# Kernel optimization log

Hardware: AMD Instinct MI355X
Metric: run time of the kernel (lower is better)

## Reference

```python
import jax, jax.numpy as jnp
import numpy as np

R = 16            # DFL bins (reg_max)
C = 80            # num classes
STRIDES = (8, 16, 32)
CONF = 0.25
IOU_T = 0.45
MAX_DET = 300
K_PRE = 1024      # fixed pre-NMS candidate count (static-shape stand-in for torch's boolean mask)
CLS_OFFSET = 4096.0  # > max image coord; class-aware NMS offset (torchvision batched_nms trick)


def setup_inputs() -> dict:
    key = jax.random.key(0)
    k0, k1, k2 = jax.random.split(key, 3)
    B, CH = 16, 4 * R + C
    return {
        "p0": jax.random.normal(k0, (B, CH, 80, 80), jnp.float32),
        "p1": jax.random.normal(k1, (B, CH, 40, 40), jnp.float32),
        "p2": jax.random.normal(k2, (B, CH, 20, 20), jnp.float32),
        "h_img": 640,
        "w_img": 640,
    }


def _decode_level(p, stride):
    # p: (B, 4R+C, H, W)
    B, _, H, W = p.shape
    box_logits = p[:, : 4 * R].reshape(B, 4, R, H * W)
    bins = jnp.arange(R, dtype=p.dtype)
    # DFLIntegral: softmax over bins, expectation -> l,t,r,b distances (in stride units)
    ltrb = jnp.einsum('bkrm,r->bkm', jax.nn.softmax(box_logits, axis=2), bins) * stride  # (B,4,HW)
    yv, xv = jnp.meshgrid(jnp.arange(H, dtype=p.dtype), jnp.arange(W, dtype=p.dtype), indexing='ij')
    cx = (xv.reshape(-1) + 0.5) * stride  # (HW,)
    cy = (yv.reshape(-1) + 0.5) * stride
    x1 = cx[None] - ltrb[:, 0]
    y1 = cy[None] - ltrb[:, 1]
    x2 = cx[None] + ltrb[:, 2]
    y2 = cy[None] + ltrb[:, 3]
    boxes = jnp.stack((x1, y1, x2, y2), axis=2)  # (B, HW, 4)
    scores = jax.nn.sigmoid(p[:, 4 * R:].reshape(B, C, H * W))  # (B, C, HW)
    smax = scores.max(axis=1)      # (B, HW)
    labels = scores.argmax(axis=1)  # (B, HW) int
    return boxes, smax, labels


def _pairwise_iou(b):
    # b: (K, 4) xyxy
    area = (b[:, 2] - b[:, 0]) * (b[:, 3] - b[:, 1])
    lt = jnp.maximum(b[:, None, :2], b[None, :, :2])
    rb = jnp.minimum(b[:, None, 2:], b[None, :, 2:])
    wh = jnp.clip(rb - lt, 0.0)
    inter = wh[..., 0] * wh[..., 1]
    return inter / (area[:, None] + area[None, :] - inter + 1e-7)


def _nms_single(boxes, smax, labels):
    # boxes (A,4), smax (A,), labels (A,)
    s = jnp.where(smax > CONF, smax, -1.0)
    sv, idx = jax.lax.top_k(s, K_PRE)          # score-sorted pre-NMS candidates
    bsel = boxes[idx]                           # (K,4)
    lsel = labels[idx]
    vsel = sv > CONF                            # candidate passes conf filter
    boff = bsel + lsel[:, None].astype(bsel.dtype) * CLS_OFFSET  # class-aware offset
    iou = _pairwise_iou(boff)
    iou = iou * (1.0 - jnp.eye(K_PRE, dtype=iou.dtype))  # no self-suppression

    def step(supp, i):
        keep_i = jnp.logical_and(~supp[i], vsel[i])
        supp = jnp.where(keep_i, supp | (iou[i] > IOU_T), supp)
        return supp, keep_i

    _, keep = jax.lax.scan(step, jnp.zeros(K_PRE, bool), jnp.arange(K_PRE))
    rank = jnp.cumsum(keep) - 1
    slot = jnp.where(keep & (rank < MAX_DET), rank, MAX_DET)  # dump overflow into dummy slot
    boxes_out = jnp.zeros((MAX_DET + 1, 4), bsel.dtype).at[slot].set(bsel)[:MAX_DET]
    scores_out = jnp.zeros((MAX_DET + 1,), sv.dtype).at[slot].set(sv)[:MAX_DET]
    labels_out = jnp.full((MAX_DET + 1,), -1, jnp.int32).at[slot].set(lsel.astype(jnp.int32))[:MAX_DET]
    n = jnp.minimum(keep.sum(), MAX_DET)
    valid_out = jnp.arange(MAX_DET) < n
    return boxes_out, scores_out, labels_out, valid_out


def reference(p0, p1, p2, h_img, w_img):
    parts = [_decode_level(p, s) for p, s in zip((p0, p1, p2), STRIDES)]
    boxes = jnp.concatenate([x[0] for x in parts], axis=1)   # (B, A, 4)
    smax = jnp.concatenate([x[1] for x in parts], axis=1)    # (B, A)
    labels = jnp.concatenate([x[2] for x in parts], axis=1)  # (B, A)
    hi = jnp.array([w_img - 1, h_img - 1, w_img - 1, h_img - 1], boxes.dtype)
    boxes = jnp.clip(boxes, 0.0, hi)
    return jax.vmap(_nms_single)(boxes, smax, labels)
```

## Files before the change

kernel.cpp:

```cpp
#include <hip/hip_runtime.h>
#include <stdint.h>

#define NR 16
#define NC 80
#define NA 8400
#define NB 16
#define KPRE 1024
#define MAXDET 300
#define CONF_T 0.25f
#define IOU_THR 0.45f

__device__ __forceinline__ float read_dim(const void* p) {
  int iv = *(const int*)p;
  return (iv > 0 && iv < (1 << 20)) ? (float)iv : *(const float*)p;
}

__device__ __forceinline__ const float* level_ptr(const float* p0, const float* p1,
                                                  const float* p2, int a, int& HW,
                                                  int& W, float& stride, int& m) {
  if (a < 6400)      { HW = 6400; W = 80; stride = 8.f;  m = a;        return p0; }
  else if (a < 8000) { HW = 1600; W = 40; stride = 16.f; m = a - 6400; return p1; }
  else               { HW = 400;  W = 20; stride = 32.f; m = a - 8000; return p2; }
}

__device__ __forceinline__ uint64_t readlane64(uint64_t v, int lane) {
  uint32_t lo = (uint32_t)__builtin_amdgcn_readlane((int)(uint32_t)v, lane);
  uint32_t hi = (uint32_t)__builtin_amdgcn_readlane((int)(uint32_t)(v >> 32), lane);
  return ((uint64_t)hi << 32) | lo;
}

__global__ __launch_bounds__(64) void k_decode(
    const float* __restrict__ p0, const float* __restrict__ p1,
    const float* __restrict__ p2, const void* __restrict__ hp,
    const void* __restrict__ wp, float4* __restrict__ boxes,
    uint32_t* __restrict__ keys, int* __restrict__ labels) {
  int aid = blockIdx.x * 64 + threadIdx.x;
  int b = aid / NA, a = aid - b * NA;
  int HW, W, m; float stride;
  const float* p = level_ptr(p0, p1, p2, a, HW, W, stride, m);
  const float* base = p + (size_t)b * (4 * NR + NC) * HW + m;

  float d[4];
#pragma unroll
  for (int k = 0; k < 4; ++k) {
    const float* bk = base + (size_t)(k * NR) * HW;
    float v[NR]; float mx = -3.4e38f;
#pragma unroll
    for (int r = 0; r < NR; ++r) { v[r] = bk[(size_t)r * HW]; mx = fmaxf(mx, v[r]); }
    float se = 0.f, sn = 0.f;
#pragma unroll
    for (int r = 0; r < NR; ++r) { float e = expf(v[r] - mx); se += e; sn += e * (float)r; }
    d[k] = sn / se * stride;
  }

  const float* bc = base + (size_t)(4 * NR) * HW;
  float ml = -3.4e38f; int mc = NC;
#pragma unroll 8
  for (int ch = 0; ch < NC; ++ch) {
    float vv = bc[(size_t)ch * HW];
    if (vv > ml) { ml = vv; mc = ch; }
  }

  int y = m / W, x = m - y * W;
  float cx = ((float)x + 0.5f) * stride, cy = ((float)y + 0.5f) * stride;
  float hx = read_dim(wp) - 1.f, hy = read_dim(hp) - 1.f;
  boxes[aid] = make_float4(fminf(fmaxf(cx - d[0], 0.f), hx),
                           fminf(fmaxf(cy - d[1], 0.f), hy),
                           fminf(fmaxf(cx + d[2], 0.f), hx),
                           fminf(fmaxf(cy + d[3], 0.f), hy));
  float smax = 1.f / (1.f + expf(-ml));
  float s = smax > CONF_T ? smax : -1.0f;
  uint32_t bt = __float_as_uint(s);
  keys[aid] = (bt & 0x80000000u) ? ~bt : (bt | 0x80000000u);
  labels[aid] = mc;
}

__global__ __launch_bounds__(1024) void k_selcomp(const uint32_t* __restrict__ keys,
                                                  uint64_t* __restrict__ cmp,
                                                  int* __restrict__ ccount) {
  __shared__ __align__(16) uint32_t skeys[NA];
  __shared__ uint32_t whist[16][256];
  __shared__ uint32_t hsum[256], ssuf[256];
  __shared__ int s_b1, s_rem, s_t16, s_cnt;
  int img = blockIdx.x, tid = threadIdx.x;
  int w = tid >> 6, lane = tid & 63;
  const uint4* kb4 = (const uint4*)(keys + (size_t)img * NA);
  for (int j = tid; j < NA / 4; j += 1024) ((uint4*)skeys)[j] = kb4[j];
  if (tid == 0) s_cnt = 0;

  for (int j = tid; j < 16 * 256; j += 1024) ((uint32_t*)whist)[j] = 0;
  __syncthreads();
  for (int j = tid; j < NA; j += 1024) atomicAdd(&whist[w][skeys[j] >> 24], 1u);
  __syncthreads();
  if (tid < 256) { uint32_t s = 0; for (int i = 0; i < 16; ++i) s += whist[i][tid]; hsum[tid] = s; }
  __syncthreads();
  if (tid < 256) { uint32_t s = 0; for (int j = tid; j < 256; ++j) s += hsum[j]; ssuf[tid] = s; }
  __syncthreads();
  if (tid < 256) {
    uint32_t ab = (tid == 255) ? 0u : ssuf[tid + 1];
    if (ssuf[tid] >= KPRE && ab < KPRE) { s_b1 = tid; s_rem = KPRE - (int)ab; }
  }
  __syncthreads();
  int b1 = s_b1, rem = s_rem;
  __syncthreads();

  for (int j = tid; j < 16 * 256; j += 1024) ((uint32_t*)whist)[j] = 0;
  __syncthreads();
  for (int j = tid; j < NA; j += 1024) {
    uint32_t k = skeys[j];
    if ((int)(k >> 24) == b1) atomicAdd(&whist[w][(k >> 16) & 0xFF], 1u);
  }
  __syncthreads();
  if (tid < 256) { uint32_t s = 0; for (int i = 0; i < 16; ++i) s += whist[i][tid]; hsum[tid] = s; }
  __syncthreads();
  if (tid < 256) { uint32_t s = 0; for (int j = tid; j < 256; ++j) s += hsum[j]; ssuf[tid] = s; }
  __syncthreads();
  if (tid < 256) {
    int ab = (tid == 255) ? 0 : (int)ssuf[tid + 1];
    if ((int)ssuf[tid] >= rem && ab < rem) s_t16 = (b1 << 8) | tid;
  }
  __syncthreads();
  uint32_t t16 = (uint32_t)s_t16;

  for (int j0 = 0; j0 < NA; j0 += 1024) {
    int j = j0 + tid;
    uint32_t k = (j < NA) ? skeys[j] : 0;
    bool pass = (j < NA) && ((k >> 16) >= t16);
    uint64_t mask = __ballot(pass);
    int pre = __popcll(mask & ((1ull << lane) - 1ull));
    int wc = __popcll(mask);
    int base = 0;
    if (lane == 0) base = wc ? atomicAdd(&s_cnt, wc) : 0;
    base = __shfl(base, 0);
    if (pass)
      cmp[(size_t)img * NA + base + pre] =
          ((uint64_t)k << 32) | (uint64_t)(0xFFFFFFFFu - (uint32_t)j);
  }
  __syncthreads();
  if (tid == 0) ccount[img] = s_cnt;
}

__global__ __launch_bounds__(256) void k_rank2(
    const uint64_t* __restrict__ cmp, const int* __restrict__ ccount,
    const float4* __restrict__ boxes, const int* __restrict__ labels,
    float4* __restrict__ selbox, float4* __restrict__ selboff,
    float* __restrict__ selscore, int* __restrict__ sellab) {
  __shared__ uint64_t sk[2048];
  int img = blockIdx.y;
  int M = ccount[img]; if (M > NA) M = NA;
  if (blockIdx.x * 256 >= M) return;
  int c = blockIdx.x * 256 + threadIdx.x;
  uint64_t kc = (c < M) ? cmp[(size_t)img * NA + c] : 0;
  int rank = 0;
  for (int j0 = 0; j0 < M; j0 += 2048) {
    int nchunk = min(2048, M - j0);
    __syncthreads();
    for (int j = threadIdx.x; j < nchunk; j += 256)
      sk[j] = cmp[(size_t)img * NA + j0 + j];
    __syncthreads();
    if (c < M) {
      int j = 0;
      for (; j + 4 <= nchunk; j += 4) {
        rank += (int)(sk[j] > kc) + (int)(sk[j + 1] > kc) +
                (int)(sk[j + 2] > kc) + (int)(sk[j + 3] > kc);
      }
      for (; j < nchunk; ++j) rank += (int)(sk[j] > kc);
    }
  }
  if (c < M && rank < KPRE) {
    int a = (int)(0xFFFFFFFFu - (uint32_t)kc);
    uint32_t uk = (uint32_t)(kc >> 32);
    uint32_t bits = (uk & 0x80000000u) ? (uk & 0x7FFFFFFFu) : ~uk;
    float s = __uint_as_float(bits);
    int lab = labels[img * NA + a];
    float4 bx = boxes[img * NA + a];
    float off = (float)lab * 4096.0f;
    int o = img * KPRE + rank;
    selbox[o] = bx;
    selboff[o] = make_float4(bx.x + off, bx.y + off, bx.z + off, bx.w + off);
    selscore[o] = s;
    sellab[o] = lab;
  }
}

__global__ __launch_bounds__(256) void k_iou(const float4* __restrict__ selboff,
                                             uint64_t* __restrict__ rowmask) {
  __shared__ float4 bb[KPRE];
  __shared__ float sar[KPRE];
  int img = blockIdx.y;
  for (int j = threadIdx.x; j < KPRE; j += 256) {
    float4 v = selboff[img * KPRE + j];
    bb[j] = v;
    sar[j] = (v.z - v.x) * (v.w - v.y);
  }
  __syncthreads();
  int i = blockIdx.x * 16 + (threadIdx.x & 15);
  int w = threadIdx.x >> 4;
  int rot = w & 3;
  float4 bi = bb[i];
  float ai = sar[i];
  uint64_t bits = 0;
  for (int jj = 0; jj < 64; ++jj) {
    int jb = (jj + rot) & 63;
    int j = w * 64 + jb;
    float4 bj = bb[j];
    float lx = fmaxf(bi.x, bj.x), ly = fmaxf(bi.y, bj.y);
    float rx = fminf(bi.z, bj.z), ry = fminf(bi.w, bj.w);
    float iw = fmaxf(rx - lx, 0.f), ih = fmaxf(ry - ly, 0.f);
    float inter = iw * ih;
    float aj = sar[j];
    float iou = inter / (ai + aj - inter + 1e-7f);
    bits |= (uint64_t)((iou > IOU_THR) && (j != i)) << jb;
  }
  rowmask[(size_t)img * 16384 + (size_t)w * 1024 + i] = bits;
}

__global__ __launch_bounds__(64) void k_scan(
    const uint64_t* __restrict__ rowmask, const float4* __restrict__ selbox,
    const float* __restrict__ selscore, const int* __restrict__ sellab,
    float* __restrict__ out) {
  __shared__ float lsc[KPRE];
  __shared__ uint64_t buf[2][16 * 65];
  __shared__ int keepidx[MAXDET];
  int img = blockIdx.x, lane = threadIdx.x;
  int wsel = lane & 15, q = lane >> 4;
  const uint64_t* g = rowmask + (size_t)img * 16384;

  for (int j = lane; j < KPRE; j += 64) lsc[j] = selscore[img * KPRE + j];

  {
    uint64_t r0[16];
#pragma unroll
    for (int t = 0; t < 16; ++t) r0[t] = g[t * 1024 + lane];
#pragma unroll
    for (int t = 0; t < 16; ++t) buf[0][t * 65 + lane] = r0[t];
  }
  asm volatile("" ::: "memory");

  uint64_t remv = 0;
  int n = 0;
  for (int c = 0; c < 16; ++c) {
    uint64_t rn[16];
    if (c + 1 < 16) {
#pragma unroll
      for (int t = 0; t < 16; ++t) rn[t] = g[t * 1024 + (c + 1) * 64 + lane];
    }
    const uint64_t* B = buf[c & 1];
    uint64_t m = B[c * 65 + lane];
    float sc = lsc[c * 64 + lane];
    uint64_t vmask = __ballot(sc > CONF_T);
    uint64_t cur = readlane64(remv, c) | readlane64(remv, c + 16) |
                   readlane64(remv, c + 32) | readlane64(remv, c + 48);
    uint64_t kmask = 0;
#pragma unroll
    for (int ii = 0; ii < 64; ++ii) {
      if (((vmask >> ii) & 1ull) && !((cur >> ii) & 1ull)) {
        cur |= readlane64(m, ii);
        kmask |= (1ull << ii);
        if (lane == 0 && n < MAXDET) keepidx[n] = c * 64 + ii;
        n++;
      }
    }
    {
      uint64_t acc = 0;
#pragma unroll
      for (int t = 0; t < 16; ++t) {
        int ii = q * 16 + t;
        uint64_t msk = (uint64_t)0 - ((kmask >> ii) & 1ull);
        acc |= B[wsel * 65 + ii] & msk;
      }
      remv |= acc;
    }
    if (!((vmask >> 63) & 1ull) || n >= MAXDET) break;
    if (c + 1 < 16) {
#pragma unroll
      for (int t = 0; t < 16; ++t) buf[(c + 1) & 1][t * 65 + lane] = rn[t];
    }
    asm volatile("" ::: "memory");
  }

  asm volatile("" ::: "memory");
  float* ob = out;
  float* os = out + NB * MAXDET * 4;
  float* ol = out + NB * MAXDET * 5;
  float* ov = out + NB * MAXDET * 6;
  int nk = n < MAXDET ? n : MAXDET;
  for (int s0 = 0; s0 < MAXDET; s0 += 64) {
    int slot = s0 + lane;
    if (slot >= MAXDET) break;
    bool v = slot < nk;
    float4 bx = make_float4(0.f, 0.f, 0.f, 0.f);
    float scv = 0.f, lbv = -1.f;
    if (v) {
      int i = keepidx[slot];
      bx = selbox[img * KPRE + i];
      scv = lsc[i];
      lbv = (float)sellab[img * KPRE + i];
    }
    ((float4*)ob)[img * MAXDET + slot] = bx;
    os[img * MAXDET + slot] = scv;
    ol[img * MAXDET + slot] = lbv;
    ov[img * MAXDET + slot] = v ? 1.0f : 0.0f;
  }
}

extern "C" void kernel_launch(void* const* d_in, const int* in_sizes, int n_in,
                              void* d_out, int out_size, void* d_ws, size_t ws_size,
                              hipStream_t stream) {
  const float* p0 = (const float*)d_in[0];
  const float* p1 = (const float*)d_in[1];
  const float* p2 = (const float*)d_in[2];
  const void* hp = d_in[3];
  const void* wp = d_in[4];

  char* ws = (char*)d_ws;
  float4*   boxes    = (float4*)(ws + 0);
  uint64_t* rowmask  = (uint64_t*)(ws + 0);
  uint32_t* keys     = (uint32_t*)(ws + 2150400);
  int*      labels   = (int*)(ws + 2688000);
  float4*   selbox   = (float4*)(ws + 3225600);
  float4*   selboff  = (float4*)(ws + 3487744);
  float*    selscore = (float*)(ws + 3749888);
  int*      sellab   = (int*)(ws + 3815424);
  int*      ccount   = (int*)(ws + 3880960);
  uint64_t* cmp      = (uint64_t*)(ws + 3881024);

  k_decode<<<(NB * NA) / 64, 64, 0, stream>>>(p0, p1, p2, hp, wp,
                                              boxes, keys, labels);
  k_selcomp<<<NB, 1024, 0, stream>>>(keys, cmp, ccount);
  dim3 rg((NA + 255) / 256, NB);
  k_rank2<<<rg, 256, 0, stream>>>(cmp, ccount, boxes, labels,
                                  selbox, selboff, selscore, sellab);
  dim3 ig(KPRE / 16, NB);
  k_iou<<<ig, 256, 0, stream>>>(selboff, rowmask);
  k_scan<<<NB, 64, 0, stream>>>(rowmask, selbox, selscore, sellab,
                                (float*)d_out);
}
```

Before: 195.2 us.

## Split per-image radix top-K selection into multi-block histogram and compaction kernels

Replaces the single 1024-thread block per image that did two radix-histogram passes and the compaction with three kernels, each launched over 16 segments per image. Partial histograms are merged with global atomics, and the candidate count is kept by a global atomic counter. The global histogram and counter are zeroed inside the decode kernel. The goal is to spread the selection work across many more CUs than 16 blocks can use, at the cost of two extra launches and global atomic traffic.

```diff
diff --git a/kernel.cpp b/kernel.cpp
--- a/kernel.cpp
+++ b/kernel.cpp
@@ -9,6 +9,7 @@
 #define MAXDET 300
 #define CONF_T 0.25f
 #define IOU_THR 0.45f
+#define SEG 525
 
 __device__ __forceinline__ float read_dim(const void* p) {
   int iv = *(const int*)p;
@@ -33,8 +34,10 @@
     const float* __restrict__ p0, const float* __restrict__ p1,
     const float* __restrict__ p2, const void* __restrict__ hp,
     const void* __restrict__ wp, float4* __restrict__ boxes,
-    uint32_t* __restrict__ keys, int* __restrict__ labels) {
+    uint32_t* __restrict__ keys, int* __restrict__ labels,
+    uint32_t* __restrict__ gz) {
   int aid = blockIdx.x * 64 + threadIdx.x;
+  if (aid < 2 * NB * 256 + 16) gz[aid] = 0;
   int b = aid / NA, a = aid - b * NA;
   int HW, W, m; float stride;
   const float* p = level_ptr(p0, p1, p2, a, HW, W, stride, m);
@@ -75,69 +78,90 @@
   labels[aid] = mc;
 }
 
-__global__ __launch_bounds__(1024) void k_selcomp(const uint32_t* __restrict__ keys,
-                                                  uint64_t* __restrict__ cmp,
-                                                  int* __restrict__ ccount) {
-  __shared__ __align__(16) uint32_t skeys[NA];
-  __shared__ uint32_t whist[16][256];
-  __shared__ uint32_t hsum[256], ssuf[256];
-  __shared__ int s_b1, s_rem, s_t16, s_cnt;
-  int img = blockIdx.x, tid = threadIdx.x;
-  int w = tid >> 6, lane = tid & 63;
-  const uint4* kb4 = (const uint4*)(keys + (size_t)img * NA);
-  for (int j = tid; j < NA / 4; j += 1024) ((uint4*)skeys)[j] = kb4[j];
-  if (tid == 0) s_cnt = 0;
-
-  for (int j = tid; j < 16 * 256; j += 1024) ((uint32_t*)whist)[j] = 0;
-  __syncthreads();
-  for (int j = tid; j < NA; j += 1024) atomicAdd(&whist[w][skeys[j] >> 24], 1u);
-  __syncthreads();
-  if (tid < 256) { uint32_t s = 0; for (int i = 0; i < 16; ++i) s += whist[i][tid]; hsum[tid] = s; }
-  __syncthreads();
-  if (tid < 256) { uint32_t s = 0; for (int j = tid; j < 256; ++j) s += hsum[j]; ssuf[tid] = s; }
-  __syncthreads();
-  if (tid < 256) {
-    uint32_t ab = (tid == 255) ? 0u : ssuf[tid + 1];
-    if (ssuf[tid] >= KPRE && ab < KPRE) { s_b1 = tid; s_rem = KPRE - (int)ab; }
+
+__global__ __launch_bounds__(256) void k_hist1(const uint32_t* __restrict__ keys,
+                                               uint32_t* __restrict__ ghist1) {
+  __shared__ uint32_t h[4][256];
+  int img = blockIdx.y, seg = blockIdx.x, tid = threadIdx.x, w = tid >> 6;
+  for (int j = tid; j < 1024; j += 256) ((uint32_t*)h)[j] = 0;
+  __syncthreads();
+  const uint32_t* kb = keys + (size_t)img * NA + seg * SEG;
+  for (int j = tid; j < SEG; j += 256) atomicAdd(&h[w][kb[j] >> 24], 1u);
+  __syncthreads();
+  uint32_t s = h[0][tid] + h[1][tid] + h[2][tid] + h[3][tid];
+  if (s) atomicAdd(&ghist1[img * 256 + tid], s);
+}
+
+__global__ __launch_bounds__(256) void k_hist2(const uint32_t* __restrict__ keys,
+                                               const uint32_t* __restrict__ ghist1,
+                                               uint32_t* __restrict__ ghist2) {
+  __shared__ uint32_t hs[256];
+  __shared__ uint32_t h[4][256];
+  __shared__ int s_b1;
+  int img = blockIdx.y, seg = blockIdx.x, tid = threadIdx.x, w = tid >> 6;
+  hs[tid] = ghist1[img * 256 + tid];
+  for (int j = tid; j < 1024; j += 256) ((uint32_t*)h)[j] = 0;
+  __syncthreads();
+  {
+    uint32_t s = 0;
+    for (int j = tid; j < 256; ++j) s += hs[j];
+    if (s >= KPRE && (s - hs[tid]) < KPRE) s_b1 = tid;
+  }
+  __syncthreads();
+  int b1 = s_b1;
+  const uint32_t* kb = keys + (size_t)img * NA + seg * SEG;
+  for (int j = tid; j < SEG; j += 256) {
+    uint32_t k = kb[j];
+    if ((int)(k >> 24) == b1) atomicAdd(&h[w][(k >> 16) & 0xFF], 1u);
+  }
+  __syncthreads();
+  uint32_t s2 = h[0][tid] + h[1][tid] + h[2][tid] + h[3][tid];
+  if (s2) atomicAdd(&ghist2[img * 256 + tid], s2);
+}
+
+__global__ __launch_bounds__(256) void k_compact(const uint32_t* __restrict__ keys,
+                                                 const uint32_t* __restrict__ ghist1,
+                                                 const uint32_t* __restrict__ ghist2,
+                                                 uint64_t* __restrict__ cmp,
+                                                 int* __restrict__ gcount) {
+  __shared__ uint32_t hs[256];
+  __shared__ int s_b1, s_rem, s_t16;
+  int img = blockIdx.y, seg = blockIdx.x, tid = threadIdx.x, lane = tid & 63;
+  hs[tid] = ghist1[img * 256 + tid];
+  __syncthreads();
+  {
+    uint32_t s = 0;
+    for (int j = tid; j < 256; ++j) s += hs[j];
+    if (s >= KPRE && (s - hs[tid]) < KPRE) { s_b1 = tid; s_rem = KPRE - (int)(s - hs[tid]); }
   }
   __syncthreads();
   int b1 = s_b1, rem = s_rem;
   __syncthreads();
-
-  for (int j = tid; j < 16 * 256; j += 1024) ((uint32_t*)whist)[j] = 0;
-  __syncthreads();
-  for (int j = tid; j < NA; j += 1024) {
-    uint32_t k = skeys[j];
-    if ((int)(k >> 24) == b1) atomicAdd(&whist[w][(k >> 16) & 0xFF], 1u);
-  }
-  __syncthreads();
-  if (tid < 256) { uint32_t s = 0; for (int i = 0; i < 16; ++i) s += whist[i][tid]; hsum[tid] = s; }
-  __syncthreads();
-  if (tid < 256) { uint32_t s = 0; for (int j = tid; j < 256; ++j) s += hsum[j]; ssuf[tid] = s; }
-  __syncthreads();
-  if (tid < 256) {
-    int ab = (tid == 255) ? 0 : (int)ssuf[tid + 1];
-    if ((int)ssuf[tid] >= rem && ab < rem) s_t16 = (b1 << 8) | tid;
+  hs[tid] = ghist2[img * 256 + tid];
+  __syncthreads();
+  {
+    uint32_t s = 0;
+    for (int j = tid; j < 256; ++j) s += hs[j];
+    if ((int)s >= rem && (int)(s - hs[tid]) < rem) s_t16 = (b1 << 8) | tid;
   }
   __syncthreads();
   uint32_t t16 = (uint32_t)s_t16;
-
-  for (int j0 = 0; j0 < NA; j0 += 1024) {
+  const uint32_t* kb = keys + (size_t)img * NA + seg * SEG;
+  for (int j0 = 0; j0 < SEG; j0 += 256) {
     int j = j0 + tid;
-    uint32_t k = (j < NA) ? skeys[j] : 0;
-    bool pass = (j < NA) && ((k >> 16) >= t16);
+    uint32_t k = (j < SEG) ? kb[j] : 0;
+    bool pass = (j < SEG) && ((k >> 16) >= t16);
     uint64_t mask = __ballot(pass);
     int pre = __popcll(mask & ((1ull << lane) - 1ull));
     int wc = __popcll(mask);
     int base = 0;
-    if (lane == 0) base = wc ? atomicAdd(&s_cnt, wc) : 0;
+    if (lane == 0) base = wc ? atomicAdd(&gcount[img], wc) : 0;
     base = __shfl(base, 0);
     if (pass)
       cmp[(size_t)img * NA + base + pre] =
-          ((uint64_t)k << 32) | (uint64_t)(0xFFFFFFFFu - (uint32_t)j);
-  }
-  __syncthreads();
-  if (tid == 0) ccount[img] = s_cnt;
+          ((uint64_t)k << 32) |
+          (uint64_t)(0xFFFFFFFFu - (uint32_t)(seg * SEG + j));
+  }
 }
 
 __global__ __launch_bounds__(256) void k_rank2(
@@ -322,14 +346,20 @@
   float4*   selboff  = (float4*)(ws + 3487744);
   float*    selscore = (float*)(ws + 3749888);
   int*      sellab   = (int*)(ws + 3815424);
-  int*      ccount   = (int*)(ws + 3880960);
   uint64_t* cmp      = (uint64_t*)(ws + 3881024);
+  uint32_t* ghist1   = (uint32_t*)(ws + 4956224);
+  uint32_t* ghist2   = (uint32_t*)(ws + 4972608);
+  int*      gcount   = (int*)(ws + 4988992);
+  uint32_t* gz       = (uint32_t*)(ws + 4956224);
 
   k_decode<<<(NB * NA) / 64, 64, 0, stream>>>(p0, p1, p2, hp, wp,
-                                              boxes, keys, labels);
-  k_selcomp<<<NB, 1024, 0, stream>>>(keys, cmp, ccount);
+                                              boxes, keys, labels, gz);
+  dim3 sg(16, NB);
+  k_hist1<<<sg, 256, 0, stream>>>(keys, ghist1);
+  k_hist2<<<sg, 256, 0, stream>>>(keys, ghist1, ghist2);
+  k_compact<<<sg, 256, 0, stream>>>(keys, ghist1, ghist2, cmp, gcount);
   dim3 rg((NA + 255) / 256, NB);
-  k_rank2<<<rg, 256, 0, stream>>>(cmp, ccount, boxes, labels,
+  k_rank2<<<rg, 256, 0, stream>>>(cmp, gcount, boxes, labels,
                                   selbox, selboff, selscore, sellab);
   dim3 ig(KPRE / 16, NB);
   k_iou<<<ig, 256, 0, stream>>>(selboff, rowmask);
```

After: 218.7 us. 1.12x slower.
